# Kernel optimization log

Hardware: AMD Instinct MI355X
Metric: run time of the kernel (lower is better)

The kernel has to match this reference:

```python
import jax, jax.numpy as jnp
import numpy as np

T, B, D = 512, 128, 512


def setup_inputs() -> dict:
    key = jax.random.key(0)
    k1, k2, k3, k4 = jax.random.split(key, 4)
    scale = 1.0 / np.sqrt(D)
    return {
        "x": jax.random.normal(k1, (T, B, D), dtype=jnp.float32),
        "dones": jax.random.randint(k2, (T, B), 0, 2).astype(jnp.bool_),
        "c0": jnp.zeros((B, D), dtype=jnp.float32),
        "h0": jnp.zeros((B, D), dtype=jnp.float32),
        "Wi": jax.random.normal(k3, (D, 4 * D), dtype=jnp.float32) * scale,
        "Wh": jax.random.normal(k4, (D, 4 * D), dtype=jnp.float32) * scale,
        "b": jnp.zeros((4 * D,), dtype=jnp.float32),
    }


def reference(x, dones, c0, h0, Wi, Wh, b):
    # Faithful translation of ScannedLSTM: scan over time; on done, reset
    # carry to zeros before applying flax OptimizedLSTMCell (gates i,f,g,o;
    # x@Wi has no bias, h@Wh + b carries the bias).
    def step(carry, xs):
        c, h = carry
        xt, dt = xs  # xt: [B, D], dt: [B] bool
        m = dt[:, None]
        c = jnp.where(m, jnp.zeros_like(c), c)
        h = jnp.where(m, jnp.zeros_like(h), h)
        z = xt @ Wi + h @ Wh + b  # [B, 4D]
        i, f, g, o = jnp.split(z, 4, axis=-1)
        i = jax.nn.sigmoid(i)
        f = jax.nn.sigmoid(f)
        g = jnp.tanh(g)
        o = jax.nn.sigmoid(o)
        new_c = f * c + i * g
        new_h = o * jnp.tanh(new_c)
        return (new_c, new_h), new_h

    (_, _), ys = jax.lax.scan(step, (c0, h0), (x, dones))
    return ys  # [T, B, D]
```

## Files before the change

### kernel.cpp

```cpp
#include <hip/hip_runtime.h>

#define TT 512
#define BB 128
#define DD 512
#define NTHR 256
#define NBLK 512
#define TAIL_S0 40

typedef _Float16 f16x8 __attribute__((ext_vector_type(8)));
typedef float f32x16 __attribute__((ext_vector_type(16)));
union H8 { f16x8 h; int4 i4; };

__device__ __forceinline__ float sigm(float v) {
  return 1.0f / (1.0f + __expf(-v));
}
__device__ __forceinline__ float tanh_fast(float v) {
  float av = fabsf(v);
  float e = __expf(-2.0f * av);
  float t = (1.0f - e) / (1.0f + e);
  return copysignf(t, v);
}
__device__ __forceinline__ unsigned short f2h(float v) {
  _Float16 h = (_Float16)v; unsigned short u; __builtin_memcpy(&u, &h, 2); return u;
}
__device__ __forceinline__ float h2f(unsigned short u) {
  _Float16 h; __builtin_memcpy(&h, &u, 2); return (float)h;
}
__device__ __forceinline__ unsigned pk2(float a, float b) {
#if __has_builtin(__builtin_amdgcn_cvt_pkrtz)
  __fp16 __attribute__((ext_vector_type(2))) p = __builtin_amdgcn_cvt_pkrtz(a, b);
  unsigned u; __builtin_memcpy(&u, &p, 4); return u;
#else
  union { _Float16 h[2]; unsigned u; } u;
  u.h[0] = (_Float16)a; u.h[1] = (_Float16)b; return u.u;
#endif
}
__device__ __forceinline__ H8 pack8(const float4& a, const float4& b) {
  H8 r;
  r.i4 = make_int4((int)pk2(a.x, a.y), (int)pk2(a.z, a.w),
                   (int)pk2(b.x, b.y), (int)pk2(b.z, b.w));
  return r;
}

__global__ void lstm_setup(const unsigned char* __restrict__ dones_raw,
                           int* __restrict__ lists,
                           int* __restrict__ counts,
                           int* __restrict__ offsets,
                           int* __restrict__ idxin)
{
  __shared__ int s_cnt[512];
  __shared__ int s_cur[512];
  __shared__ int s_isbool;
  const int tid = threadIdx.x;
  if (tid == 0) s_isbool = 0;
  for (int i = tid; i < 512; i += 256) s_cnt[i] = 0;
  __syncthreads();
  int loc = 0;
  for (int i = tid; i < TT * BB; i += 256)
    if ((i & 3) && dones_raw[i]) { loc = 1; break; }
  if (loc) atomicOr(&s_isbool, 1);
  __syncthreads();
  const int isBool = s_isbool;
  const int* d32 = (const int*)dones_raw;
  if (tid < BB) {
    int a = 0;
    for (int t = 0; t < TT; ++t) {
      const int idx = t * BB + tid;
      const int dn = isBool ? (int)dones_raw[idx] : d32[idx];
      a = (t == 0) ? 0 : (dn ? 0 : a + 1);
      atomicAdd(&s_cnt[a], 1);
    }
  }
  __syncthreads();
  if (tid == 0) {
    int acc = 0;
    for (int i = 0; i < 512; ++i) {
      counts[i] = s_cnt[i]; offsets[i] = acc; s_cur[i] = acc; acc += s_cnt[i];
    }
  }
  __syncthreads();
  if (tid < BB) {
    int a = 0;
    for (int t = 0; t < TT; ++t) {
      const int idx = t * BB + tid;
      const int dn = isBool ? (int)dones_raw[idx] : d32[idx];
      a = (t == 0) ? 0 : (dn ? 0 : a + 1);
      const int slot = atomicAdd(&s_cur[a], 1);
      lists[slot] = idx;
      idxin[idx] = slot - offsets[a];
    }
  }
}

__global__ void lstm_pack(const float* __restrict__ Wi,
                          const float* __restrict__ Wh,
                          unsigned short* __restrict__ Wpack)
{
  const int gid = blockIdx.x * blockDim.x + threadIdx.x;
  const int lane = gid & 63;
  const int kstep = (gid >> 6) & 63;
  const int F = gid >> 12;
  const int m = lane & 31, kq = lane >> 5;
  const int gate = m >> 3;
  const int col = gate * 512 + F * 8 + (m & 7);
  union { _Float16 hh[8]; int4 i4; } u;
#pragma unroll
  for (int e = 0; e < 8; ++e) {
    const int k = kstep * 16 + kq * 8 + e;
    const float v = (k < 512) ? Wi[(size_t)k * 2048 + col]
                              : Wh[(size_t)(k - 512) * 2048 + col];
    u.hh[e] = (_Float16)v;
  }
  *(int4*)(Wpack + (size_t)gid * 8) = u.i4;
}

__device__ __forceinline__ void do_tile(
    const float* __restrict__ x,
    const char* __restrict__ Wlds,
    const float4 Bi, const float4 Bf, const float4 Bg, const float4 Bo,
    const int* __restrict__ lists,
    const int* __restrict__ idxin,
    float* __restrict__ out,
    unsigned short* __restrict__ Ccur,
    const unsigned short* __restrict__ Cprev,
    int s, int M, int off, int rt, int cbs)
{
  const int tid = threadIdx.x;
  const int lane = tid & 63;
  const int wv = tid >> 6;
  const int n = lane & 31, hi = lane >> 5;
  const int dbase = cbs * 8 + 4 * hi;

  const int rbase = rt * 256 + wv * 64 + n;
  const int p0 = (rbase < M) ? lists[off + rbase] : -1;
  const int p1 = (rbase + 32 < M) ? lists[off + rbase + 32] : -1;
  const float* xp0 = x + (size_t)(p0 >= 0 ? p0 : 0) * DD;
  const float* xp1 = x + (size_t)(p1 >= 0 ? p1 : 0) * DD;

  f32x16 acc0 = {};
  f32x16 acc1 = {};

  float4 la0, la1, lb0, lb1;
  {
    const int kk = hi * 8;
    la0 = *(const float4*)(xp0 + kk); la1 = *(const float4*)(xp0 + kk + 4);
    lb0 = *(const float4*)(xp1 + kk); lb1 = *(const float4*)(xp1 + kk + 4);
  }

#pragma unroll 2
  for (int ks = 0; ks < 32; ++ks) {
    H8 f0 = pack8(la0, la1);
    H8 f1 = pack8(lb0, lb1);
    if (ks + 1 < 32) {
      const int kk = (ks + 1) * 16 + hi * 8;
      la0 = *(const float4*)(xp0 + kk); la1 = *(const float4*)(xp0 + kk + 4);
      lb0 = *(const float4*)(xp1 + kk); lb1 = *(const float4*)(xp1 + kk + 4);
    }
    H8 aw; aw.i4 = *(const int4*)(Wlds + (size_t)ks * 1024 + lane * 16);
    acc0 = __builtin_amdgcn_mfma_f32_32x32x16_f16(aw.h, f0.h, acc0, 0, 0, 0);
    acc1 = __builtin_amdgcn_mfma_f32_32x32x16_f16(aw.h, f1.h, acc1, 0, 0, 0);
  }

  if (s > 0) {
    const float* hp0 = out + (size_t)((p0 >= 0 ? p0 : BB) - BB) * DD;
    const float* hp1 = out + (size_t)((p1 >= 0 ? p1 : BB) - BB) * DD;
    {
      const int kk = hi * 8;
      la0 = *(const float4*)(hp0 + kk); la1 = *(const float4*)(hp0 + kk + 4);
      lb0 = *(const float4*)(hp1 + kk); lb1 = *(const float4*)(hp1 + kk + 4);
    }
#pragma unroll 2
    for (int ks2 = 0; ks2 < 32; ++ks2) {
      H8 f0 = pack8(la0, la1);
      H8 f1 = pack8(lb0, lb1);
      if (ks2 + 1 < 32) {
        const int kk = (ks2 + 1) * 16 + hi * 8;
        la0 = *(const float4*)(hp0 + kk); la1 = *(const float4*)(hp0 + kk + 4);
        lb0 = *(const float4*)(hp1 + kk); lb1 = *(const float4*)(hp1 + kk + 4);
      }
      H8 aw; aw.i4 = *(const int4*)(Wlds + (size_t)(32 + ks2) * 1024 + lane * 16);
      acc0 = __builtin_amdgcn_mfma_f32_32x32x16_f16(aw.h, f0.h, acc0, 0, 0, 0);
      acc1 = __builtin_amdgcn_mfma_f32_32x32x16_f16(aw.h, f1.h, acc1, 0, 0, 0);
    }
  }

#pragma unroll
  for (int b = 0; b < 2; ++b) {
    const int p = b ? p1 : p0;
    if (p < 0) continue;
    const f32x16 A = b ? acc1 : acc0;
    ushort4 cin4 = make_ushort4(0, 0, 0, 0);
    if (s > 0) {
      const int slotp = idxin[p - BB];
      cin4 = *(const ushort4*)(Cprev + (size_t)slotp * DD + dbase);
    }
    const int slotc = idxin[p];
    float hres[4]; unsigned short cres[4];
#pragma unroll
    for (int r = 0; r < 4; ++r) {
      const unsigned short cb16 = (r == 0) ? cin4.x : (r == 1) ? cin4.y
                                : (r == 2) ? cin4.z : cin4.w;
      const float cin = h2f(cb16);
      const float zi = A[r]      + ((r == 0) ? Bi.x : (r == 1) ? Bi.y : (r == 2) ? Bi.z : Bi.w);
      const float zf = A[4 + r]  + ((r == 0) ? Bf.x : (r == 1) ? Bf.y : (r == 2) ? Bf.z : Bf.w);
      const float zg = A[8 + r]  + ((r == 0) ? Bg.x : (r == 1) ? Bg.y : (r == 2) ? Bg.z : Bg.w);
      const float zo = A[12 + r] + ((r == 0) ? Bo.x : (r == 1) ? Bo.y : (r == 2) ? Bo.z : Bo.w);
      const float iv = sigm(zi), fv = sigm(zf);
      const float gv = tanh_fast(zg), ov = sigm(zo);
      const float cn = fv * cin + iv * gv;
      cres[r] = f2h(cn);
      hres[r] = ov * tanh_fast(cn);
    }
    *(float4*)(out + (size_t)p * DD + dbase) =
        make_float4(hres[0], hres[1], hres[2], hres[3]);
    *(ushort4*)(Ccur + (size_t)slotc * DD + dbase) =
        make_ushort4(cres[0], cres[1], cres[2], cres[3]);
  }
}

__global__ __launch_bounds__(NTHR) void lstm_step(
    const float* __restrict__ x, const unsigned short* __restrict__ Wp,
    const float* __restrict__ bias, const int* __restrict__ lists,
    const int* __restrict__ counts, const int* __restrict__ offsets,
    const int* __restrict__ idxin, float* __restrict__ out,
    char* __restrict__ Cregion, int s)
{
  const int M = counts[s];
  if (M == 0) return;
  const int bid = blockIdx.x;
  const int rtg = bid & 7;
  const int cbs = bid >> 3;
  const int rowTiles = (M + 255) >> 8;
  if (rtg >= rowTiles) return;

  __shared__ __align__(16) char Wlds[65536];
  {
    const int4* src = (const int4*)((const char*)Wp + (size_t)cbs * 65536);
    int4* dst = (int4*)Wlds;
    for (int i = threadIdx.x; i < 4096; i += NTHR) dst[i] = src[i];
  }
  __syncthreads();

  const int lane = threadIdx.x & 63;
  const int hi = lane >> 5;
  const int dbase = cbs * 8 + 4 * hi;
  const float4 Bi = *(const float4*)(bias + dbase);
  const float4 Bf = *(const float4*)(bias + 512 + dbase);
  const float4 Bg = *(const float4*)(bias + 1024 + dbase);
  const float4 Bo = *(const float4*)(bias + 1536 + dbase);
  const int M0 = counts[0];
  unsigned short* Cb = (unsigned short*)Cregion;
  const int off = offsets[s];
  unsigned short* Ccur = Cb + ((s & 1) ? (size_t)M0 * DD : 0);
  const unsigned short* Cprev = Cb + ((s & 1) ? 0 : (size_t)M0 * DD);
  for (int rt = rtg; rt < rowTiles; rt += 8)
    do_tile(x, Wlds, Bi, Bf, Bg, Bo, lists, idxin, out, Ccur, Cprev,
            s, M, off, rt, cbs);
}

__global__ void lstm_tail(
    const float* __restrict__ x, const float* __restrict__ Wi,
    const float* __restrict__ Wh, const float* __restrict__ bias,
    const int* __restrict__ lists, const int* __restrict__ counts,
    const int* __restrict__ offsets, const int* __restrict__ idxin,
    float* __restrict__ out, char* __restrict__ Cregion)
{
  const int d = threadIdx.x;
  const int M0 = counts[0];
  unsigned short* CbufE = (unsigned short*)Cregion;
  for (int s = TAIL_S0; s < TT; ++s) {
    const int M = counts[s];
    if (M == 0) return;
    unsigned short* Ccur = CbufE + ((s & 1) ? (size_t)M0 * DD : 0);
    const unsigned short* Cprev = CbufE + ((s & 1) ? 0 : (size_t)M0 * DD);
    for (int mI = 0; mI < M; ++mI) {
      const int p = lists[offsets[s] + mI];
      const float* xp = x + (size_t)p * DD;
      const float* hp = out + (size_t)(p - BB) * DD;
      float zi = bias[d], zf = bias[512 + d], zg = bias[1024 + d], zo = bias[1536 + d];
      for (int k = 0; k < DD; ++k) {
        const float xv = xp[k], hv = hp[k];
        const size_t rk = (size_t)k * 2048;
        zi += xv * Wi[rk + d]        + hv * Wh[rk + d];
        zf += xv * Wi[rk + 512 + d]  + hv * Wh[rk + 512 + d];
        zg += xv * Wi[rk + 1024 + d] + hv * Wh[rk + 1024 + d];
        zo += xv * Wi[rk + 1536 + d] + hv * Wh[rk + 1536 + d];
      }
      const float cin = h2f(((const unsigned short*)Cprev)[(size_t)idxin[p - BB] * DD + d]);
      const float iv = sigm(zi), fv = sigm(zf), gv = tanh_fast(zg), ov = sigm(zo);
      const float cn = fv * cin + iv * gv;
      ((unsigned short*)Ccur)[(size_t)idxin[p] * DD + d] = f2h(cn);
      out[(size_t)p * DD + d] = ov * tanh_fast(cn);
    }
    __syncthreads();
  }
}

extern "C" void kernel_launch(void* const* d_in, const int* in_sizes, int n_in,
                              void* d_out, int out_size, void* d_ws, size_t ws_size,
                              hipStream_t stream) {
  const float* x = (const float*)d_in[0];
  const unsigned char* dones = (const unsigned char*)d_in[1];
  const float* Wi   = (const float*)d_in[4];
  const float* Wh   = (const float*)d_in[5];
  const float* bias = (const float*)d_in[6];
  float* out = (float*)d_out;

  char* ws = (char*)d_ws;
  int* counts           = (int*)(ws);
  int* offsets          = (int*)(ws + 2048);
  int* idxin            = (int*)(ws + 4096);
  int* lists            = (int*)(ws + 266240);
  unsigned short* Wpack = (unsigned short*)(ws + 528384);
  char* Cregion         = ws + 4722688;

  lstm_setup<<<1, 256, 0, stream>>>(dones, lists, counts, offsets, idxin);
  lstm_pack<<<1024, 256, 0, stream>>>(Wi, Wh, Wpack);

  for (int s = 0; s < TAIL_S0; ++s)
    lstm_step<<<NBLK, NTHR, 0, stream>>>(x, Wpack, bias, lists, counts,
                                         offsets, idxin, out, Cregion, s);
  lstm_tail<<<1, 512, 0, stream>>>(x, Wi, Wh, bias, lists, counts,
                                   offsets, idxin, out, Cregion);
}
```

Measured before the change: 2.382 ms.

## Use 8 waves per block with one row group each and deeper prefetch

Doubles the block size from 256 to 512 threads so each wave handles 32 rows with one accumulator, where before it handled 64 rows with two. The K loop is restructured to prefetch 64-column chunks into two register buffers and issue four MFMAs per chunk. The x-phase prefetch is chained straight into the h-phase loads. Bias loads move into the epilogue and launch bounds request 4 blocks per CU. The intent is more waves in flight and better latency hiding for the global B-operand loads. The cost is more register pressure per thread and each wave reusing an LDS weight fragment for half as many rows.

Measured after the change: 3.436 ms. 44.2% more time.

```diff
diff --git a/kernel.cpp b/kernel.cpp
--- a/kernel.cpp
+++ b/kernel.cpp
@@ -3,7 +3,7 @@
 #define TT 512
 #define BB 128
 #define DD 512
-#define NTHR 256
+#define NTHR 512
 #define NBLK 512
 #define TAIL_S0 40
 
@@ -114,10 +114,33 @@
   *(int4*)(Wpack + (size_t)gid * 8) = u.i4;
 }
 
+__device__ __forceinline__ void load_b8(const float* __restrict__ src, int kk0,
+                                        float4* __restrict__ buf) {
+#pragma unroll
+  for (int j = 0; j < 4; ++j) {
+    buf[2 * j]     = *(const float4*)(src + kk0 + j * 16);
+    buf[2 * j + 1] = *(const float4*)(src + kk0 + j * 16 + 4);
+  }
+}
+__device__ __forceinline__ void packb(const float4* __restrict__ buf,
+                                      H8* __restrict__ c) {
+#pragma unroll
+  for (int j = 0; j < 4; ++j) c[j] = pack8(buf[2 * j], buf[2 * j + 1]);
+}
+__device__ __forceinline__ void mfma4c(f32x16& acc, const char* __restrict__ Wl,
+                                       int ksbase, int lane,
+                                       const H8* __restrict__ c) {
+#pragma unroll
+  for (int j = 0; j < 4; ++j) {
+    H8 aw; aw.i4 = *(const int4*)(Wl + (size_t)(ksbase + j) * 1024 + lane * 16);
+    acc = __builtin_amdgcn_mfma_f32_32x32x16_f16(aw.h, c[j].h, acc, 0, 0, 0);
+  }
+}
+
 __device__ __forceinline__ void do_tile(
     const float* __restrict__ x,
     const char* __restrict__ Wlds,
-    const float4 Bi, const float4 Bf, const float4 Bg, const float4 Bo,
+    const float* __restrict__ bias,
     const int* __restrict__ lists,
     const int* __restrict__ idxin,
     float* __restrict__ out,
@@ -131,64 +154,48 @@
   const int n = lane & 31, hi = lane >> 5;
   const int dbase = cbs * 8 + 4 * hi;
 
-  const int rbase = rt * 256 + wv * 64 + n;
-  const int p0 = (rbase < M) ? lists[off + rbase] : -1;
-  const int p1 = (rbase + 32 < M) ? lists[off + rbase + 32] : -1;
-  const float* xp0 = x + (size_t)(p0 >= 0 ? p0 : 0) * DD;
-  const float* xp1 = x + (size_t)(p1 >= 0 ? p1 : 0) * DD;
-
-  f32x16 acc0 = {};
-  f32x16 acc1 = {};
-
-  float4 la0, la1, lb0, lb1;
-  {
-    const int kk = hi * 8;
-    la0 = *(const float4*)(xp0 + kk); la1 = *(const float4*)(xp0 + kk + 4);
-    lb0 = *(const float4*)(xp1 + kk); lb1 = *(const float4*)(xp1 + kk + 4);
-  }
-
-#pragma unroll 2
-  for (int ks = 0; ks < 32; ++ks) {
-    H8 f0 = pack8(la0, la1);
-    H8 f1 = pack8(lb0, lb1);
-    if (ks + 1 < 32) {
-      const int kk = (ks + 1) * 16 + hi * 8;
-      la0 = *(const float4*)(xp0 + kk); la1 = *(const float4*)(xp0 + kk + 4);
-      lb0 = *(const float4*)(xp1 + kk); lb1 = *(const float4*)(xp1 + kk + 4);
-    }
-    H8 aw; aw.i4 = *(const int4*)(Wlds + (size_t)ks * 1024 + lane * 16);
-    acc0 = __builtin_amdgcn_mfma_f32_32x32x16_f16(aw.h, f0.h, acc0, 0, 0, 0);
-    acc1 = __builtin_amdgcn_mfma_f32_32x32x16_f16(aw.h, f1.h, acc1, 0, 0, 0);
+  const int rr = rt * 256 + wv * 32 + n;
+  const int p = (rr < M) ? lists[off + rr] : -1;
+  const float* xs = x + (size_t)(p >= 0 ? p : 0) * DD + hi * 8;
+  const float* hs = out + (size_t)((p >= 0 ? p : BB) - BB) * DD + hi * 8;
+
+  f32x16 acc = {};
+  float4 bufA[8], bufB[8];
+  H8 c[4];
+
+  load_b8(xs, 0, bufA);
+  load_b8(xs, 64, bufB);
+
+#pragma unroll
+  for (int bb = 0; bb < 8; bb += 2) {
+    packb(bufA, c);
+    if (bb < 6)      load_b8(xs, (bb + 2) * 64, bufA);
+    else if (s > 0)  load_b8(hs, 0, bufA);
+    mfma4c(acc, Wlds, 4 * bb, lane, c);
+    packb(bufB, c);
+    if (bb < 6)      load_b8(xs, (bb + 3) * 64, bufB);
+    else if (s > 0)  load_b8(hs, 64, bufB);
+    mfma4c(acc, Wlds, 4 * bb + 4, lane, c);
   }
 
   if (s > 0) {
-    const float* hp0 = out + (size_t)((p0 >= 0 ? p0 : BB) - BB) * DD;
-    const float* hp1 = out + (size_t)((p1 >= 0 ? p1 : BB) - BB) * DD;
-    {
-      const int kk = hi * 8;
-      la0 = *(const float4*)(hp0 + kk); la1 = *(const float4*)(hp0 + kk + 4);
-      lb0 = *(const float4*)(hp1 + kk); lb1 = *(const float4*)(hp1 + kk + 4);
-    }
-#pragma unroll 2
-    for (int ks2 = 0; ks2 < 32; ++ks2) {
-      H8 f0 = pack8(la0, la1);
-      H8 f1 = pack8(lb0, lb1);
-      if (ks2 + 1 < 32) {
-        const int kk = (ks2 + 1) * 16 + hi * 8;
-        la0 = *(const float4*)(hp0 + kk); la1 = *(const float4*)(hp0 + kk + 4);
-        lb0 = *(const float4*)(hp1 + kk); lb1 = *(const float4*)(hp1 + kk + 4);
-      }
-      H8 aw; aw.i4 = *(const int4*)(Wlds + (size_t)(32 + ks2) * 1024 + lane * 16);
-      acc0 = __builtin_amdgcn_mfma_f32_32x32x16_f16(aw.h, f0.h, acc0, 0, 0, 0);
-      acc1 = __builtin_amdgcn_mfma_f32_32x32x16_f16(aw.h, f1.h, acc1, 0, 0, 0);
-    }
-  }
-
-#pragma unroll
-  for (int b = 0; b < 2; ++b) {
-    const int p = b ? p1 : p0;
-    if (p < 0) continue;
-    const f32x16 A = b ? acc1 : acc0;
+    const char* Wh2 = Wlds + 32 * 1024;
+#pragma unroll
+    for (int bb = 0; bb < 8; bb += 2) {
+      packb(bufA, c);
+      if (bb < 6) load_b8(hs, (bb + 2) * 64, bufA);
+      mfma4c(acc, Wh2, 4 * bb, lane, c);
+      packb(bufB, c);
+      if (bb < 6) load_b8(hs, (bb + 3) * 64, bufB);
+      mfma4c(acc, Wh2, 4 * bb + 4, lane, c);
+    }
+  }
+
+  if (p >= 0) {
+    const float4 Bi = *(const float4*)(bias + dbase);
+    const float4 Bf = *(const float4*)(bias + 512 + dbase);
+    const float4 Bg = *(const float4*)(bias + 1024 + dbase);
+    const float4 Bo = *(const float4*)(bias + 1536 + dbase);
     ushort4 cin4 = make_ushort4(0, 0, 0, 0);
     if (s > 0) {
       const int slotp = idxin[p - BB];
@@ -201,10 +208,10 @@
       const unsigned short cb16 = (r == 0) ? cin4.x : (r == 1) ? cin4.y
                                 : (r == 2) ? cin4.z : cin4.w;
       const float cin = h2f(cb16);
-      const float zi = A[r]      + ((r == 0) ? Bi.x : (r == 1) ? Bi.y : (r == 2) ? Bi.z : Bi.w);
-      const float zf = A[4 + r]  + ((r == 0) ? Bf.x : (r == 1) ? Bf.y : (r == 2) ? Bf.z : Bf.w);
-      const float zg = A[8 + r]  + ((r == 0) ? Bg.x : (r == 1) ? Bg.y : (r == 2) ? Bg.z : Bg.w);
-      const float zo = A[12 + r] + ((r == 0) ? Bo.x : (r == 1) ? Bo.y : (r == 2) ? Bo.z : Bo.w);
+      const float zi = acc[r]      + ((r == 0) ? Bi.x : (r == 1) ? Bi.y : (r == 2) ? Bi.z : Bi.w);
+      const float zf = acc[4 + r]  + ((r == 0) ? Bf.x : (r == 1) ? Bf.y : (r == 2) ? Bf.z : Bf.w);
+      const float zg = acc[8 + r]  + ((r == 0) ? Bg.x : (r == 1) ? Bg.y : (r == 2) ? Bg.z : Bg.w);
+      const float zo = acc[12 + r] + ((r == 0) ? Bo.x : (r == 1) ? Bo.y : (r == 2) ? Bo.z : Bo.w);
       const float iv = sigm(zi), fv = sigm(zf);
       const float gv = tanh_fast(zg), ov = sigm(zo);
       const float cn = fv * cin + iv * gv;
@@ -218,7 +225,7 @@
   }
 }
 
-__global__ __launch_bounds__(NTHR) void lstm_step(
+__global__ __launch_bounds__(NTHR, 4) void lstm_step(
     const float* __restrict__ x, const unsigned short* __restrict__ Wp,
     const float* __restrict__ bias, const int* __restrict__ lists,
     const int* __restrict__ counts, const int* __restrict__ offsets,
@@ -241,20 +248,13 @@
   }
   __syncthreads();
 
-  const int lane = threadIdx.x & 63;
-  const int hi = lane >> 5;
-  const int dbase = cbs * 8 + 4 * hi;
-  const float4 Bi = *(const float4*)(bias + dbase);
-  const float4 Bf = *(const float4*)(bias + 512 + dbase);
-  const float4 Bg = *(const float4*)(bias + 1024 + dbase);
-  const float4 Bo = *(const float4*)(bias + 1536 + dbase);
   const int M0 = counts[0];
   unsigned short* Cb = (unsigned short*)Cregion;
   const int off = offsets[s];
   unsigned short* Ccur = Cb + ((s & 1) ? (size_t)M0 * DD : 0);
   const unsigned short* Cprev = Cb + ((s & 1) ? 0 : (size_t)M0 * DD);
   for (int rt = rtg; rt < rowTiles; rt += 8)
-    do_tile(x, Wlds, Bi, Bf, Bg, Bo, lists, idxin, out, Ccur, Cprev,
+    do_tile(x, Wlds, bias, lists, idxin, out, Ccur, Cprev,
             s, M, off, rt, cbs);
 }
 
```
